# Optimization experiments

Hardware: AMD Instinct MI355X
Metric: run time of the kernel (lower is better)

Reference implementation:

```python
import jax, jax.numpy as jnp
import numpy as np

# ReRAM crossbar constants (from init_kwargs)
GMAX = 0.000333
GMIN = 3.33e-07
DELTA_G = GMAX - GMIN
VDD = 3.3
N_LVL_V = 256
DELTA_V = VDD / (N_LVL_V - 1)
CRXB_COL, CRXB_ROW, CRXB_SIZE = 16, 16, 64
BATCH = 4096


def setup_inputs() -> dict:
    key = jax.random.key(0)
    k1, k2 = jax.random.split(key)
    inputs = jax.random.normal(k1, (BATCH, 1, CRXB_ROW, CRXB_SIZE, 1), dtype=jnp.float32)
    weight = jax.random.normal(k2, (CRXB_COL, CRXB_ROW, CRXB_SIZE, CRXB_SIZE), dtype=jnp.float32)
    nchout_index = jnp.arange(CRXB_COL * CRXB_SIZE, dtype=jnp.int64)
    return {"inputs": inputs, "weight": weight, "nchout_index": nchout_index}


def reference(inputs, weight, nchout_index):
    # DAC: scale digital input to voltage
    input_crxb = inputs * DELTA_V                      # [N,1,row,S,1]
    # w2g: map signed weight to positive/negative conductance crossbars
    g_pos = GMIN + jax.nn.relu(weight) * DELTA_G       # [col,row,S,S]
    g_neg = GMIN + jax.nn.relu(-weight) * DELTA_G
    # split pos/neg crossbar matmuls (broadcast over batch), fused subtract
    out = jnp.matmul(g_pos, input_crxb) - jnp.matmul(g_neg, input_crxb)  # [N,col,row,S,1]
    out = jnp.swapaxes(out, 2, 3)                      # [N,col,S,row,1]
    n = out.shape[0]
    out = out.reshape(n, CRXB_COL * CRXB_SIZE, CRXB_ROW, 1)
    out = jnp.take(out, nchout_index, axis=1)          # output channel select
    return jnp.squeeze(out, axis=-1)                   # [N, col*S, row]
```

## Files before the change

kernel.cpp:

```cpp
#include <hip/hip_runtime.h>
#include <hip/hip_bf16.h>
#include <stdint.h>


using bf16x8 = __attribute__((ext_vector_type(8))) short;
using f32x4  = __attribute__((ext_vector_type(4))) float;
using f32x2  = __attribute__((ext_vector_type(2))) float;

#define NPT 16
#define NIT 16
#define PITCH_B 2064
#define BUFB 33024
#define LDS_BYTES (2*BUFB)

#define BARRIER() asm volatile("s_waitcnt lgkmcnt(0)\n\ts_barrier" ::: "memory")

__device__ inline bf16x8 cvt8v(float4 a, float4 b) {
  union { bf16x8 v; __hip_bfloat162 h[4]; } r;
  r.h[0] = __float22bfloat162_rn(float2{a.x, a.y});
  r.h[1] = __float22bfloat162_rn(float2{a.z, a.w});
  r.h[2] = __float22bfloat162_rn(float2{b.x, b.y});
  r.h[3] = __float22bfloat162_rn(float2{b.z, b.w});
  return r.v;
}

__global__ __launch_bounds__(512, 4)
void crxb_kernel(const float* __restrict__ X, const float* __restrict__ W,
                 float* __restrict__ out) {
  extern __shared__ char smem[];
  const int t   = threadIdx.x;
  const int bid = blockIdx.x;
  const int ngrp = ((bid & 7) << 1) | ((bid >> 3) & 1);
  const int mt   = bid >> 4;
  const int c  = mt >> 1;
  const int i0 = (mt & 1) << 5;
  const int m0 = mt << 5;

  const int wid = t >> 6;
  const int l   = t & 63;
  const int lr  = l & 15;
  const int lk  = l >> 4;
  const int r0w = wid << 1;

  const float S = (float)((0.000333 - 3.33e-07) * (3.3 / 255.0));

  bf16x8 A[2][2][2];
  #pragma unroll
  for (int rr = 0; rr < 2; ++rr)
    #pragma unroll
    for (int ks = 0; ks < 2; ++ks)
      #pragma unroll
      for (int a = 0; a < 2; ++a) {
        const float* gw = W + (((size_t)(c * 16 + r0w + rr) * 64) + (i0 + a * 16 + lr)) * 64
                            + ks * 32 + lk * 8;
        float4 wa = *(const float4*)gw;
        float4 wb = *(const float4*)(gw + 4);
        wa.x *= S; wa.y *= S; wa.z *= S; wa.w *= S;
        wb.x *= S; wb.y *= S; wb.z *= S; wb.w *= S;
        A[rr][ks][a] = cvt8v(wa, wb);
      }

  {
    #pragma unroll
    for (int p = 0; p < 4; ++p) {
      int u = p * 512 + t;
      int n = u >> 7, r = (u >> 3) & 15, k8 = u & 7;
      const float* gx = X + (((size_t)(ngrp * 256 + n) * 16) + r) * 64 + k8 * 8;
      *(bf16x8*)(smem + (size_t)n * PITCH_B + r * 128 + k8 * 16) =
          cvt8v(*(const float4*)gx, *(const float4*)(gx + 4));
    }
  }
  BARRIER();

  int cur = 0;
  for (int it = 0; it < NIT; ++it) {
    char* bufc = smem + cur * BUFB;
    char* bufn = smem + (cur ^ 1) * BUFB;
    const int n0 = ngrp * 256 + it * NPT;

    float4 xp[8];
    if (it + 1 < NIT) {
      #pragma unroll
      for (int p = 0; p < 4; ++p) {
        int u = p * 512 + t;
        int n = u >> 7, r = (u >> 3) & 15, k8 = u & 7;
        const float* gx = X + (((size_t)(n0 + NPT + n) * 16) + r) * 64 + k8 * 8;
        xp[2 * p]     = *(const float4*)gx;
        xp[2 * p + 1] = *(const float4*)(gx + 4);
      }
    }

    f32x4 acc[2][2];
    #pragma unroll
    for (int rr = 0; rr < 2; ++rr)
      #pragma unroll
      for (int a = 0; a < 2; ++a) acc[rr][a] = (f32x4){0.f, 0.f, 0.f, 0.f};

    #pragma unroll
    for (int rr = 0; rr < 2; ++rr) {
      const int r = r0w + rr;
      #pragma unroll
      for (int ks = 0; ks < 2; ++ks) {
        bf16x8 Bf = *(const bf16x8*)(bufc + (size_t)lr * PITCH_B + r * 128 + ks * 64 + lk * 16);
        acc[rr][0] = __builtin_amdgcn_mfma_f32_16x16x32_bf16(A[rr][ks][0], Bf, acc[rr][0], 0, 0, 0);
        acc[rr][1] = __builtin_amdgcn_mfma_f32_16x16x32_bf16(A[rr][ks][1], Bf, acc[rr][1], 0, 0, 0);
      }
    }
    BARRIER();

    #pragma unroll
    for (int a = 0; a < 2; ++a)
      #pragma unroll
      for (int reg = 0; reg < 4; ++reg) {
        f32x2 v = {acc[0][a][reg], acc[1][a][reg]};
        const int mm = a * 16 + lk * 4 + reg;
        *(f32x2*)(bufc + ((size_t)lr * 516 + mm * 16 + r0w) * 4) = v;
      }
    BARRIER();

    {
      const int n  = t >> 5;
      const int j0 = t & 31;
      const float* Or = (const float*)(bufc + (size_t)n * PITCH_B);
      float* gout = out + ((size_t)(n0 + n)) * 16384 + (size_t)m0 * 16;
      #pragma unroll
      for (int q = 0; q < 4; ++q) {
        const int u = (q * 32 + j0) * 4;
        f32x4 v = *(const f32x4*)(Or + u);
        __builtin_nontemporal_store(v, (f32x4*)(gout + u));
      }
    }

    if (it + 1 < NIT) {
      #pragma unroll
      for (int p = 0; p < 4; ++p) {
        int u = p * 512 + t;
        int n = u >> 7, r = (u >> 3) & 15, k8 = u & 7;
        *(bf16x8*)(bufn + (size_t)n * PITCH_B + r * 128 + k8 * 16) = cvt8v(xp[2 * p], xp[2 * p + 1]);
      }
    }
    BARRIER();
    cur ^= 1;
  }
}

extern "C" void kernel_launch(void* const* d_in, const int* in_sizes, int n_in,
                              void* d_out, int out_size, void* d_ws, size_t ws_size,
                              hipStream_t stream) {
  const float* X = (const float*)d_in[0];
  const float* W = (const float*)d_in[1];
  float* out = (float*)d_out;
  (void)in_sizes; (void)n_in; (void)d_ws; (void)ws_size; (void)out_size;

  (void)hipFuncSetAttribute(reinterpret_cast<const void*>(crxb_kernel),
                            hipFuncAttributeMaxDynamicSharedMemorySize, LDS_BYTES);

  crxb_kernel<<<dim3(512), dim3(512), LDS_BYTES, stream>>>(X, W, out);
}
```

Measured before the change: 59.56 us.

## Drop LDS double buffering and double grid size for higher occupancy

Removes the double-buffered LDS staging and register prefetch of the next input tile, so each block uses a single buffer and loads the next tile synchronously. Batch groups are halved to 128 samples per block and the grid doubles to 1024 blocks, with launch bounds raised to allow 8 blocks per CU. The aim is to hide latency through more concurrent waves rather than software pipelining. In exchange, global loads no longer overlap compute within a block, an extra barrier is added per iteration, and each block reloads its weights for half as much batch work.

```diff
diff --git a/kernel.cpp b/kernel.cpp
--- a/kernel.cpp
+++ b/kernel.cpp
@@ -8,10 +8,10 @@
 using f32x2  = __attribute__((ext_vector_type(2))) float;
 
 #define NPT 16
-#define NIT 16
+#define NIT 8
 #define PITCH_B 2064
-#define BUFB 33024
-#define LDS_BYTES (2*BUFB)
+#define BUFB (16 * PITCH_B)
+#define LDS_BYTES BUFB
 
 #define BARRIER() asm volatile("s_waitcnt lgkmcnt(0)\n\ts_barrier" ::: "memory")
 
@@ -24,14 +24,15 @@
   return r.v;
 }
 
-__global__ __launch_bounds__(512, 4)
+__global__ __launch_bounds__(512, 8)
 void crxb_kernel(const float* __restrict__ X, const float* __restrict__ W,
                  float* __restrict__ out) {
   extern __shared__ char smem[];
   const int t   = threadIdx.x;
   const int bid = blockIdx.x;
-  const int ngrp = ((bid & 7) << 1) | ((bid >> 3) & 1);
-  const int mt   = bid >> 4;
+  const int xcd  = bid & 7;
+  const int ng   = xcd * 4 + ((bid >> 3) & 3);
+  const int mt   = bid >> 5;
   const int c  = mt >> 1;
   const int i0 = (mt & 1) << 5;
   const int m0 = mt << 5;
@@ -65,30 +66,15 @@
     for (int p = 0; p < 4; ++p) {
       int u = p * 512 + t;
       int n = u >> 7, r = (u >> 3) & 15, k8 = u & 7;
-      const float* gx = X + (((size_t)(ngrp * 256 + n) * 16) + r) * 64 + k8 * 8;
+      const float* gx = X + (((size_t)(ng * 128 + n) * 16) + r) * 64 + k8 * 8;
       *(bf16x8*)(smem + (size_t)n * PITCH_B + r * 128 + k8 * 16) =
           cvt8v(*(const float4*)gx, *(const float4*)(gx + 4));
     }
   }
   BARRIER();
 
-  int cur = 0;
   for (int it = 0; it < NIT; ++it) {
-    char* bufc = smem + cur * BUFB;
-    char* bufn = smem + (cur ^ 1) * BUFB;
-    const int n0 = ngrp * 256 + it * NPT;
-
-    float4 xp[8];
-    if (it + 1 < NIT) {
-      #pragma unroll
-      for (int p = 0; p < 4; ++p) {
-        int u = p * 512 + t;
-        int n = u >> 7, r = (u >> 3) & 15, k8 = u & 7;
-        const float* gx = X + (((size_t)(n0 + NPT + n) * 16) + r) * 64 + k8 * 8;
-        xp[2 * p]     = *(const float4*)gx;
-        xp[2 * p + 1] = *(const float4*)(gx + 4);
-      }
-    }
+    const int n0 = ng * 128 + it * NPT;
 
     f32x4 acc[2][2];
     #pragma unroll
@@ -101,7 +87,7 @@
       const int r = r0w + rr;
       #pragma unroll
       for (int ks = 0; ks < 2; ++ks) {
-        bf16x8 Bf = *(const bf16x8*)(bufc + (size_t)lr * PITCH_B + r * 128 + ks * 64 + lk * 16);
+        bf16x8 Bf = *(const bf16x8*)(smem + (size_t)lr * PITCH_B + r * 128 + ks * 64 + lk * 16);
         acc[rr][0] = __builtin_amdgcn_mfma_f32_16x16x32_bf16(A[rr][ks][0], Bf, acc[rr][0], 0, 0, 0);
         acc[rr][1] = __builtin_amdgcn_mfma_f32_16x16x32_bf16(A[rr][ks][1], Bf, acc[rr][1], 0, 0, 0);
       }
@@ -114,14 +100,14 @@
       for (int reg = 0; reg < 4; ++reg) {
         f32x2 v = {acc[0][a][reg], acc[1][a][reg]};
         const int mm = a * 16 + lk * 4 + reg;
-        *(f32x2*)(bufc + ((size_t)lr * 516 + mm * 16 + r0w) * 4) = v;
+        *(f32x2*)(smem + ((size_t)lr * 516 + mm * 16 + r0w) * 4) = v;
       }
     BARRIER();
 
     {
       const int n  = t >> 5;
       const int j0 = t & 31;
-      const float* Or = (const float*)(bufc + (size_t)n * PITCH_B);
+      const float* Or = (const float*)(smem + (size_t)n * PITCH_B);
       float* gout = out + ((size_t)(n0 + n)) * 16384 + (size_t)m0 * 16;
       #pragma unroll
       for (int q = 0; q < 4; ++q) {
@@ -132,15 +118,17 @@
     }
 
     if (it + 1 < NIT) {
+      BARRIER();
       #pragma unroll
       for (int p = 0; p < 4; ++p) {
         int u = p * 512 + t;
         int n = u >> 7, r = (u >> 3) & 15, k8 = u & 7;
-        *(bf16x8*)(bufn + (size_t)n * PITCH_B + r * 128 + k8 * 16) = cvt8v(xp[2 * p], xp[2 * p + 1]);
+        const float* gx = X + (((size_t)(n0 + NPT + n) * 16) + r) * 64 + k8 * 8;
+        *(bf16x8*)(smem + (size_t)n * PITCH_B + r * 128 + k8 * 16) =
+            cvt8v(*(const float4*)gx, *(const float4*)(gx + 4));
       }
+      BARRIER();
     }
-    BARRIER();
-    cur ^= 1;
   }
 }
 
@@ -155,5 +143,5 @@
   (void)hipFuncSetAttribute(reinterpret_cast<const void*>(crxb_kernel),
                             hipFuncAttributeMaxDynamicSharedMemorySize, LDS_BYTES);
 
-  crxb_kernel<<<dim3(512), dim3(512), LDS_BYTES, stream>>>(X, W, out);
+  crxb_kernel<<<dim3(1024), dim3(512), LDS_BYTES, stream>>>(X, W, out);
 }
```

After: 108.0 us. +81.4%, slower.

## Double block size to 1024 threads with one crossbar row per wave

Applied to the files above, without the earlier changes.

Doubles the threads per block from 512 to 1024, so each of 16 waves handles a single crossbar row instead of two. Per-thread register state (weights, accumulators, prefetch buffers) is halved, and the load, store and LDS loops are reindexed to match. The aim is more wave-level parallelism to hide latency in this memory-bound kernel. In exchange there are more threads taking part in each barrier and narrower per-thread LDS writes (scalar floats instead of float2).

```diff
diff --git a/kernel.cpp b/kernel.cpp
--- a/kernel.cpp
+++ b/kernel.cpp
@@ -5,7 +5,6 @@
 
 using bf16x8 = __attribute__((ext_vector_type(8))) short;
 using f32x4  = __attribute__((ext_vector_type(4))) float;
-using f32x2  = __attribute__((ext_vector_type(2))) float;
 
 #define NPT 16
 #define NIT 16
@@ -24,7 +23,7 @@
   return r.v;
 }
 
-__global__ __launch_bounds__(512, 4)
+__global__ __launch_bounds__(1024, 8)
 void crxb_kernel(const float* __restrict__ X, const float* __restrict__ W,
                  float* __restrict__ out) {
   extern __shared__ char smem[];
@@ -40,30 +39,27 @@
   const int l   = t & 63;
   const int lr  = l & 15;
   const int lk  = l >> 4;
-  const int r0w = wid << 1;
 
   const float S = (float)((0.000333 - 3.33e-07) * (3.3 / 255.0));
 
-  bf16x8 A[2][2][2];
+  bf16x8 A[2][2];
   #pragma unroll
-  for (int rr = 0; rr < 2; ++rr)
+  for (int ks = 0; ks < 2; ++ks)
     #pragma unroll
-    for (int ks = 0; ks < 2; ++ks)
-      #pragma unroll
-      for (int a = 0; a < 2; ++a) {
-        const float* gw = W + (((size_t)(c * 16 + r0w + rr) * 64) + (i0 + a * 16 + lr)) * 64
-                            + ks * 32 + lk * 8;
-        float4 wa = *(const float4*)gw;
-        float4 wb = *(const float4*)(gw + 4);
-        wa.x *= S; wa.y *= S; wa.z *= S; wa.w *= S;
-        wb.x *= S; wb.y *= S; wb.z *= S; wb.w *= S;
-        A[rr][ks][a] = cvt8v(wa, wb);
-      }
+    for (int a = 0; a < 2; ++a) {
+      const float* gw = W + (((size_t)(c * 16 + wid) * 64) + (i0 + a * 16 + lr)) * 64
+                          + ks * 32 + lk * 8;
+      float4 wa = *(const float4*)gw;
+      float4 wb = *(const float4*)(gw + 4);
+      wa.x *= S; wa.y *= S; wa.z *= S; wa.w *= S;
+      wb.x *= S; wb.y *= S; wb.z *= S; wb.w *= S;
+      A[ks][a] = cvt8v(wa, wb);
+    }
 
   {
     #pragma unroll
-    for (int p = 0; p < 4; ++p) {
-      int u = p * 512 + t;
+    for (int p = 0; p < 2; ++p) {
+      int u = p * 1024 + t;
       int n = u >> 7, r = (u >> 3) & 15, k8 = u & 7;
       const float* gx = X + (((size_t)(ngrp * 256 + n) * 16) + r) * 64 + k8 * 8;
       *(bf16x8*)(smem + (size_t)n * PITCH_B + r * 128 + k8 * 16) =
@@ -78,11 +74,11 @@
     char* bufn = smem + (cur ^ 1) * BUFB;
     const int n0 = ngrp * 256 + it * NPT;
 
-    float4 xp[8];
+    float4 xp[4];
     if (it + 1 < NIT) {
       #pragma unroll
-      for (int p = 0; p < 4; ++p) {
-        int u = p * 512 + t;
+      for (int p = 0; p < 2; ++p) {
+        int u = p * 1024 + t;
         int n = u >> 7, r = (u >> 3) & 15, k8 = u & 7;
         const float* gx = X + (((size_t)(n0 + NPT + n) * 16) + r) * 64 + k8 * 8;
         xp[2 * p]     = *(const float4*)gx;
@@ -90,21 +86,15 @@
       }
     }
 
-    f32x4 acc[2][2];
-    #pragma unroll
-    for (int rr = 0; rr < 2; ++rr)
-      #pragma unroll
-      for (int a = 0; a < 2; ++a) acc[rr][a] = (f32x4){0.f, 0.f, 0.f, 0.f};
+    f32x4 acc[2];
+    acc[0] = (f32x4){0.f, 0.f, 0.f, 0.f};
+    acc[1] = (f32x4){0.f, 0.f, 0.f, 0.f};
 
     #pragma unroll
-    for (int rr = 0; rr < 2; ++rr) {
-      const int r = r0w + rr;
-      #pragma unroll
-      for (int ks = 0; ks < 2; ++ks) {
-        bf16x8 Bf = *(const bf16x8*)(bufc + (size_t)lr * PITCH_B + r * 128 + ks * 64 + lk * 16);
-        acc[rr][0] = __builtin_amdgcn_mfma_f32_16x16x32_bf16(A[rr][ks][0], Bf, acc[rr][0], 0, 0, 0);
-        acc[rr][1] = __builtin_amdgcn_mfma_f32_16x16x32_bf16(A[rr][ks][1], Bf, acc[rr][1], 0, 0, 0);
-      }
+    for (int ks = 0; ks < 2; ++ks) {
+      bf16x8 Bf = *(const bf16x8*)(bufc + (size_t)lr * PITCH_B + wid * 128 + ks * 64 + lk * 16);
+      acc[0] = __builtin_amdgcn_mfma_f32_16x16x32_bf16(A[ks][0], Bf, acc[0], 0, 0, 0);
+      acc[1] = __builtin_amdgcn_mfma_f32_16x16x32_bf16(A[ks][1], Bf, acc[1], 0, 0, 0);
     }
     BARRIER();
 
@@ -112,20 +102,19 @@
     for (int a = 0; a < 2; ++a)
       #pragma unroll
       for (int reg = 0; reg < 4; ++reg) {
-        f32x2 v = {acc[0][a][reg], acc[1][a][reg]};
         const int mm = a * 16 + lk * 4 + reg;
-        *(f32x2*)(bufc + ((size_t)lr * 516 + mm * 16 + r0w) * 4) = v;
+        *(float*)(bufc + ((size_t)lr * 516 + mm * 16 + wid) * 4) = acc[a][reg];
       }
     BARRIER();
 
     {
-      const int n  = t >> 5;
-      const int j0 = t & 31;
+      const int n  = wid;
+      const int j0 = l;
       const float* Or = (const float*)(bufc + (size_t)n * PITCH_B);
       float* gout = out + ((size_t)(n0 + n)) * 16384 + (size_t)m0 * 16;
       #pragma unroll
-      for (int q = 0; q < 4; ++q) {
-        const int u = (q * 32 + j0) * 4;
+      for (int q = 0; q < 2; ++q) {
+        const int u = (q * 64 + j0) * 4;
         f32x4 v = *(const f32x4*)(Or + u);
         __builtin_nontemporal_store(v, (f32x4*)(gout + u));
       }
@@ -133,8 +122,8 @@
 
     if (it + 1 < NIT) {
       #pragma unroll
-      for (int p = 0; p < 4; ++p) {
-        int u = p * 512 + t;
+      for (int p = 0; p < 2; ++p) {
+        int u = p * 1024 + t;
         int n = u >> 7, r = (u >> 3) & 15, k8 = u & 7;
         *(bf16x8*)(bufn + (size_t)n * PITCH_B + r * 128 + k8 * 16) = cvt8v(xp[2 * p], xp[2 * p + 1]);
       }
@@ -155,5 +144,5 @@
   (void)hipFuncSetAttribute(reinterpret_cast<const void*>(crxb_kernel),
                             hipFuncAttributeMaxDynamicSharedMemorySize, LDS_BYTES);
 
-  crxb_kernel<<<dim3(512), dim3(512), LDS_BYTES, stream>>>(X, W, out);
+  crxb_kernel<<<dim3(512), dim3(1024), LDS_BYTES, stream>>>(X, W, out);
 }
```

Result: slower. 97.65 us (+64.0%).
